# Kernel tuning notes

Measured on AMD Instinct MI355X. Metric: run time of the kernel, lower is better.

Reference implementation:

```python
import jax, jax.numpy as jnp
import numpy as np

N = 100000   # nodes
E = 1000000  # edges
IN, HID, OUT = 128, 64, 64


def setup_inputs() -> dict:
    key = jax.random.key(0)
    ks = jax.random.split(key, 6)
    x = jax.random.normal(ks[0], (N, IN), dtype=jnp.float32)
    edge_index = jax.random.randint(ks[1], (2, E), 0, N, dtype=jnp.int64)
    edge_attr = jax.random.uniform(ks[2], (E,), dtype=jnp.float32)
    # Glorot-style init like PyG GCNConv (weight [in, out], bias zeros)
    W1 = jax.random.normal(ks[3], (IN, HID), dtype=jnp.float32) * (1.0 / np.sqrt(IN))
    b1 = jnp.zeros((HID,), dtype=jnp.float32)
    W2 = jax.random.normal(ks[4], (HID, OUT), dtype=jnp.float32) * (1.0 / np.sqrt(HID))
    b2 = jnp.zeros((OUT,), dtype=jnp.float32)
    return {"x": x, "edge_index": edge_index, "edge_attr": edge_attr,
            "W1": W1, "b1": b1, "W2": W2, "b2": b2}


def gcn_conv(x, edge_index, edge_weight, W, b):
    """GCNConv: add self-loops, symmetric normalization, linear + scatter-add."""
    n = x.shape[0]
    row, col = edge_index[0], edge_index[1]
    loop = jnp.arange(n, dtype=row.dtype)
    row = jnp.concatenate([row, loop])
    col = jnp.concatenate([col, loop])
    w = jnp.concatenate([edge_weight, jnp.ones((n,), dtype=x.dtype)])
    deg = jax.ops.segment_sum(w, col, num_segments=n)              # [N]
    dinv = jnp.where(deg > 0, jax.lax.rsqrt(deg), 0.0)
    norm = dinv[row] * w * dinv[col]                               # [E+N]
    h = x @ W                                                      # [N, out]
    agg = jax.ops.segment_sum(h[row] * norm[:, None], col, num_segments=n)
    return agg + b


def reference(x, edge_index, edge_attr, W1, b1, W2, b2):
    h = jax.nn.relu(gcn_conv(x, edge_index, edge_attr, W1, b1))
    return jax.nn.relu(gcn_conv(h, edge_index, edge_attr, W2, b2))
```

## Files before the change

kernel.cpp:

```cpp
#include <hip/hip_runtime.h>


#define BNODES 512
#define LB 9
#define MAXBKT 256
#define EPT 16
#define EPB (256 * EPT)

typedef __attribute__((ext_vector_type(8))) short bf16x8;
typedef __attribute__((ext_vector_type(8))) unsigned short u16x8;
typedef __attribute__((ext_vector_type(8))) float f32x8;
typedef __attribute__((ext_vector_type(4))) float f32x4;

__device__ __forceinline__ unsigned short f2bf(float f) {
    unsigned u = __float_as_uint(f);
    u = (u + 0x7FFF + ((u >> 16) & 1)) >> 16;
    return (unsigned short)u;
}
__device__ __forceinline__ float bf2f(unsigned short h) {
    return __uint_as_float(((unsigned)h) << 16);
}
__device__ __forceinline__ f32x8 bf8tof(u16x8 u) {
    f32x8 r;
    #pragma unroll
    for (int i = 0; i < 8; ++i) r[i] = bf2f(u[i]);
    return r;
}

__device__ __forceinline__ int waveIncScan(int v, int lane) {
    #pragma unroll
    for (int d = 1; d < 64; d <<= 1) {
        int u = __shfl_up(v, d, 64);
        if (lane >= d) v += u;
    }
    return v;
}

template<int NW>
__device__ __forceinline__ int blockIncScan(int v, int t, int* wt) {
    int lane = t & 63, w = t >> 6;
    int s = waveIncScan(v, lane);
    if (lane == 63) wt[w] = s;
    __syncthreads();
    int add = 0;
    #pragma unroll
    for (int i = 0; i < NW - 1; ++i) if (i < w) add += wt[i];
    return s + add;
}

__device__ __forceinline__ f32x8 gather8(
    const unsigned short* __restrict__ G, const int2* __restrict__ sedge,
    int s, int m, int p8, f32x8 a0)
{
    f32x8 a1 = (f32x8)0.f;
    int e = s, e_end = s + m;
    if ((((unsigned long long)(sedge + e)) & 8) && e < e_end) {
        int2 pk = sedge[e++];
        float w = __int_as_float(pk.y);
        a0 += w * bf8tof(*(const u16x8*)&G[(size_t)pk.x * 64 + p8 * 8]);
    }
    for (; e + 1 < e_end; e += 2) {
        int4 pp = *(const int4*)&sedge[e];
        float w0 = __int_as_float(pp.y);
        float w1 = __int_as_float(pp.w);
        u16x8 g0 = *(const u16x8*)&G[(size_t)pp.x * 64 + p8 * 8];
        u16x8 g1 = *(const u16x8*)&G[(size_t)pp.z * 64 + p8 * 8];
        a0 += w0 * bf8tof(g0);
        a1 += w1 * bf8tof(g1);
    }
    if (e < e_end) {
        int2 pk = sedge[e];
        float w = __int_as_float(pk.y);
        a0 += w * bf8tof(*(const u16x8*)&G[(size_t)pk.x * 64 + p8 * 8]);
    }
    return a0 + a1;
}


__global__ __launch_bounds__(256) void hist_kernel(
    const int* __restrict__ col, int* __restrict__ H, int E, int NBKT,
    const float* __restrict__ W1, const float* __restrict__ W2,
    unsigned short* __restrict__ WT1, unsigned short* __restrict__ WT2, int NEB)
{
    int t = threadIdx.x, blk = blockIdx.x;
    if (blk >= NEB) {
        int i = (blk - NEB) * 256 + t;
        if (i < 64 * 128) {
            int c = i >> 7, k = i & 127;
            WT1[i] = f2bf(W1[k * 64 + c]);
        } else if (i < 64 * 128 + 64 * 64) {
            int j = i - 64 * 128;
            int c = j >> 6, k = j & 63;
            WT2[j] = f2bf(W2[k * 64 + c]);
        }
        return;
    }
    __shared__ int h[MAXBKT];
    for (int b = t; b < NBKT; b += 256) h[b] = 0;
    __syncthreads();
    int base = blk * EPB;
    #pragma unroll
    for (int i = 0; i < EPT; ++i) {
        int e = base + i * 256 + t;
        if (e < E) atomicAdd(&h[col[e] >> LB], 1);
    }
    __syncthreads();
    for (int b = t; b < NBKT; b += 256) H[blk * NBKT + b] = h[b];
}

__global__ __launch_bounds__(256) void rowscan_kernel(
    int* __restrict__ H, int* __restrict__ rowSum, int NEB, int NBKT)
{
    __shared__ int wt[4];
    int b = blockIdx.x, t = threadIdx.x;
    int v = (t < NEB) ? H[t * NBKT + b] : 0;
    int incl = blockIncScan<4>(v, t, wt);
    if (t < NEB) H[t * NBKT + b] = incl - v;
    if (t == 255) rowSum[b] = incl;
}

__global__ __launch_bounds__(256) void bktscan_kernel(
    const int* __restrict__ rowSum, int* __restrict__ bktStart, int NBKT)
{
    __shared__ int wt[4];
    int t = threadIdx.x;
    int v = (t < NBKT) ? rowSum[t] : 0;
    int incl = blockIncScan<4>(v, t, wt);
    if (t < NBKT) bktStart[t] = incl - v;
    if (t == NBKT - 1) bktStart[NBKT] = incl;
}

#define SMEMSZ (EPB * 8 + EPB + MAXBKT * 16 + 32)
__global__ __launch_bounds__(256) void scatter_gemm_kernel(
    const int* __restrict__ row, const int* __restrict__ col,
    const float* __restrict__ w, const int* __restrict__ H,
    const int* __restrict__ bktStart, int2* __restrict__ sedge1,
    int E, int NBKT, int NEB,
    const float* __restrict__ X, const unsigned short* __restrict__ WT,
    unsigned short* __restrict__ G, int n)
{
    __shared__ __align__(16) char smem[SMEMSZ];
    const int t = threadIdx.x;
    const int blk = blockIdx.x;

    if (blk < NEB) {
        int2* stage = (int2*)smem;
        unsigned char* bstage = (unsigned char*)(stage + EPB);
        int* lcnt  = (int*)(bstage + EPB);
        int* loff  = lcnt + MAXBKT;
        int* lcur  = loff + MAXBKT;
        int* gbase = lcur + MAXBKT;
        int* wt    = gbase + MAXBKT;

        for (int b = t; b < NBKT; b += 256) lcnt[b] = 0;
        __syncthreads();
        int base = blk * EPB;
        #pragma unroll
        for (int i = 0; i < EPT; ++i) {
            int e = base + i * 256 + t;
            if (e < E) atomicAdd(&lcnt[col[e] >> LB], 1);
        }
        __syncthreads();
        int v = (t < NBKT) ? lcnt[t] : 0;
        int incl = blockIncScan<4>(v, t, wt);
        if (t < NBKT) {
            int x0 = incl - v;
            loff[t] = x0;
            lcur[t] = x0;
            gbase[t] = bktStart[t] + H[blk * NBKT + t];
        }
        __syncthreads();
        #pragma unroll
        for (int i = 0; i < EPT; ++i) {
            int e = base + i * 256 + t;
            if (e < E) {
                int c = col[e];
                int b = c >> LB;
                int pos = atomicAdd(&lcur[b], 1);
                int2 pk;
                pk.x = row[e] | ((c & (BNODES - 1)) << 20);
                pk.y = __float_as_int(w[e]);
                stage[pos] = pk;
                bstage[pos] = (unsigned char)b;
            }
        }
        __syncthreads();
        int ecnt = E - base; if (ecnt > EPB) ecnt = EPB;
        for (int i = t; i < ecnt; i += 256) {
            int b = bstage[i];
            int g = gbase[b] + (i - loff[b]);
            sedge1[g] = stage[i];
        }
        return;
    }

    constexpr int K = 128, ROWB = 256, SLOTS = 16, CPR = 32;
    char* xs = smem;
    char* ws = smem + 64 * ROWB;
    const int nodeBase = (blk - NEB) * 64;

    for (int q = t; q < 64 * SLOTS; q += 256) {
        int r = q / SLOTS, s = q % SLOTS;
        uint4 v = *(const uint4*)(WT + r * K + s * 8);
        *(uint4*)(ws + r * ROWB + ((s ^ (r & 7)) * 16)) = v;
    }
    for (int q = t; q < 64 * CPR; q += 256) {
        int r = q / CPR, c = q % CPR;
        int node = nodeBase + r;
        float4 v = make_float4(0.f, 0.f, 0.f, 0.f);
        if (node < n) v = *(const float4*)(X + (size_t)node * K + c * 4);
        ushort4 h;
        h.x = f2bf(v.x); h.y = f2bf(v.y); h.z = f2bf(v.z); h.w = f2bf(v.w);
        *(ushort4*)(xs + r * ROWB + (((c >> 1) ^ (r & 7)) * 16) + (c & 1) * 8) = h;
    }
    __syncthreads();

    const int lane = t & 63;
    const int wv = t >> 6;
    const int lr = lane & 15;
    const int lk = lane >> 4;
    const int arow = (wv << 4) + lr;

    f32x4 acc[4] = {};
    #pragma unroll
    for (int kb = 0; kb < 4; ++kb) {
        int s = kb * 4 + lk;
        bf16x8 a = *(bf16x8*)(xs + arow * ROWB + ((s ^ (arow & 7)) * 16));
        #pragma unroll
        for (int cb = 0; cb < 4; ++cb) {
            int c = cb * 16 + lr;
            bf16x8 b = *(bf16x8*)(ws + c * ROWB + ((s ^ (c & 7)) * 16));
            acc[cb] = __builtin_amdgcn_mfma_f32_16x16x32_bf16(a, b, acc[cb], 0, 0, 0);
        }
    }

    int rowbase = nodeBase + (wv << 4) + (lk << 2);
    #pragma unroll
    for (int j = 0; j < 4; ++j) {
        int node = rowbase + j;
        if (node >= n) continue;
        #pragma unroll
        for (int cb = 0; cb < 4; ++cb)
            G[(size_t)node * 64 + cb * 16 + lr] = f2bf(acc[cb][j]);
    }
}

__global__ __launch_bounds__(512) void fine_kernel(
    const int2* __restrict__ sedge1, const int* __restrict__ bktStart,
    int2* __restrict__ sedge2, int* __restrict__ nodeStart,
    int* __restrict__ nodeCnt, float* __restrict__ dinv,
    unsigned short* __restrict__ g1, int n)
{
    __shared__ int cnt[BNODES];
    __shared__ float wsum[BNODES];
    __shared__ int off[BNODES];
    __shared__ int cur[BNODES];
    __shared__ float dloc[BNODES];
    __shared__ int wt[8];
    int b = blockIdx.x, t = threadIdx.x;
    cnt[t] = 0; wsum[t] = 1.0f;
    __syncthreads();
    int s = bktStart[b], e = bktStart[b + 1];
    for (int j = s + t; j < e; j += 512) {
        int2 pk = sedge1[j];
        int ld = pk.x >> 20;
        atomicAdd(&cnt[ld], 1);
        atomicAdd(&wsum[ld], __int_as_float(pk.y));
    }
    __syncthreads();
    int v = cnt[t];
    int incl = blockIncScan<8>(v, t, wt);
    int x0 = s + incl - v;
    off[t] = x0;
    cur[t] = x0;
    dloc[t] = rsqrtf(wsum[t]);
    __syncthreads();
    int node = b * BNODES + t;
    if (node < n) {
        nodeStart[node] = off[t];
        nodeCnt[node] = cnt[t];
        dinv[node] = dloc[t];
    }
    for (int j = s + t; j < e; j += 512) {
        int2 pk = sedge1[j];
        int ld = pk.x >> 20;
        int pos = atomicAdd(&cur[ld], 1);
        sedge2[pos] = make_int2(pk.x & 0xFFFFF, pk.y);
    }
    for (int q = t; q < BNODES * 8; q += 512) {
        int r = q >> 3, cc = q & 7;
        int nd = b * BNODES + r;
        if (nd >= n) continue;
        float dv = dloc[r];
        size_t offb = (size_t)nd * 64 + cc * 8;
        ushort4 u0 = *(const ushort4*)(g1 + offb);
        ushort4 u1 = *(const ushort4*)(g1 + offb + 4);
        u0.x = f2bf(bf2f(u0.x) * dv); u0.y = f2bf(bf2f(u0.y) * dv);
        u0.z = f2bf(bf2f(u0.z) * dv); u0.w = f2bf(bf2f(u0.w) * dv);
        u1.x = f2bf(bf2f(u1.x) * dv); u1.y = f2bf(bf2f(u1.y) * dv);
        u1.z = f2bf(bf2f(u1.z) * dv); u1.w = f2bf(bf2f(u1.w) * dv);
        *(ushort4*)(g1 + offb) = u0;
        *(ushort4*)(g1 + offb + 4) = u1;
    }
}

__global__ __launch_bounds__(256) void aggmm_kernel(
    const unsigned short* __restrict__ G1, const int2* __restrict__ sedge2,
    const int* __restrict__ nodeStart, const int* __restrict__ nodeCnt,
    const float* __restrict__ dinv, const float* __restrict__ bias,
    const unsigned short* __restrict__ WT2, unsigned short* __restrict__ G2, int n)
{
    constexpr int BN = 32;
    constexpr int ROWB = 128;
    __shared__ char smem[(BN + 64) * ROWB];
    char* xs = smem;
    char* ws = smem + BN * ROWB;
    const int tid = threadIdx.x;
    const int nodeBase = blockIdx.x * BN;

    for (int q = tid; q < 64 * 8; q += 256) {
        int r = q >> 3, s = q & 7;
        uint4 v = *(const uint4*)(WT2 + r * 64 + s * 8);
        *(uint4*)(ws + r * ROWB + ((s ^ (r & 7)) * 16)) = v;
    }

    int p8 = tid & 7;
    int r = tid >> 3;
    int node = nodeBase + r;
    f32x8 o = (f32x8)0.f;
    if (node < n) {
        f32x8 a = bf8tof(*(const u16x8*)&G1[(size_t)node * 64 + p8 * 8]);
        a = gather8(G1, sedge2, nodeStart[node], nodeCnt[node], p8, a);
        float di = dinv[node];
        #pragma unroll
        for (int i = 0; i < 8; ++i)
            o[i] = fmaxf(fmaf(di, a[i], bias[p8 * 8 + i]), 0.f);
    }
    u16x8 h;
    #pragma unroll
    for (int i = 0; i < 8; ++i) h[i] = f2bf(o[i]);
    *(u16x8*)(xs + r * ROWB + ((p8 ^ (r & 7)) * 16)) = h;
    __syncthreads();

    const int lane = tid & 63;
    const int w = tid >> 6;
    const int lr = lane & 15;
    const int lk = lane >> 4;
    const int rb = w >> 1;
    const int arow = rb * 16 + lr;

    f32x4 acc[2] = {};
    #pragma unroll
    for (int kb = 0; kb < 2; ++kb) {
        int s = kb * 4 + lk;
        bf16x8 a = *(bf16x8*)(xs + arow * ROWB + ((s ^ (arow & 7)) * 16));
        #pragma unroll
        for (int cc = 0; cc < 2; ++cc) {
            int c = ((w & 1) * 2 + cc) * 16 + lr;
            bf16x8 b = *(bf16x8*)(ws + c * ROWB + ((s ^ (c & 7)) * 16));
            acc[cc] = __builtin_amdgcn_mfma_f32_16x16x32_bf16(a, b, acc[cc], 0, 0, 0);
        }
    }

    int rowbase = nodeBase + rb * 16 + (lk << 2);
    #pragma unroll
    for (int j = 0; j < 4; ++j) {
        int nd = rowbase + j;
        if (nd >= n) continue;
        float dv = dinv[nd];
        #pragma unroll
        for (int cc = 0; cc < 2; ++cc)
            G2[(size_t)nd * 64 + ((w & 1) * 2 + cc) * 16 + lr] = f2bf(acc[cc][j] * dv);
    }
}

__global__ __launch_bounds__(256) void agg_kernel(
    const unsigned short* __restrict__ G, const int2* __restrict__ sedge2,
    const int* __restrict__ nodeStart, const int* __restrict__ nodeCnt,
    const float* __restrict__ dinv, const float* __restrict__ bias,
    float* __restrict__ OUT, int n)
{
    int t = blockIdx.x * blockDim.x + threadIdx.x;
    if (t >= n * 8) return;
    int node = t >> 3, p8 = t & 7;

    f32x8 a = bf8tof(*(const u16x8*)&G[(size_t)node * 64 + p8 * 8]);
    a = gather8(G, sedge2, nodeStart[node], nodeCnt[node], p8, a);

    float di = dinv[node];
    float4 o0, o1;
    o0.x = fmaxf(fmaf(di, a[0], bias[p8 * 8 + 0]), 0.f);
    o0.y = fmaxf(fmaf(di, a[1], bias[p8 * 8 + 1]), 0.f);
    o0.z = fmaxf(fmaf(di, a[2], bias[p8 * 8 + 2]), 0.f);
    o0.w = fmaxf(fmaf(di, a[3], bias[p8 * 8 + 3]), 0.f);
    o1.x = fmaxf(fmaf(di, a[4], bias[p8 * 8 + 4]), 0.f);
    o1.y = fmaxf(fmaf(di, a[5], bias[p8 * 8 + 5]), 0.f);
    o1.z = fmaxf(fmaf(di, a[6], bias[p8 * 8 + 6]), 0.f);
    o1.w = fmaxf(fmaf(di, a[7], bias[p8 * 8 + 7]), 0.f);
    *(float4*)&OUT[(size_t)node * 64 + p8 * 8] = o0;
    *(float4*)&OUT[(size_t)node * 64 + p8 * 8 + 4] = o1;
}

extern "C" void kernel_launch(void* const* d_in, const int* in_sizes, int n_in,
                              void* d_out, int out_size, void* d_ws, size_t ws_size,
                              hipStream_t stream) {
    const float* x     = (const float*)d_in[0];
    const int*   eidx  = (const int*)d_in[1];
    const float* eattr = (const float*)d_in[2];
    const float* W1    = (const float*)d_in[3];
    const float* b1    = (const float*)d_in[4];
    const float* W2    = (const float*)d_in[5];
    const float* b2    = (const float*)d_in[6];
    float* out = (float*)d_out;

    const int n = in_sizes[0] / 128;
    const int E = in_sizes[2];
    const int* row = eidx;
    const int* col = eidx + E;

    const int NBKT = (n + BNODES - 1) / BNODES;
    const int NEB  = (E + EPB - 1) / EPB;

    int2*  sedge1 = (int2*)d_ws;
    int2*  sedge2 = sedge1 + (size_t)E;
    unsigned short* g1 = (unsigned short*)(sedge2 + (size_t)E);
    unsigned short* g2 = g1 + (size_t)n * 64;
    unsigned short* WT1 = g2 + (size_t)n * 64;
    unsigned short* WT2 = WT1 + 64 * 128;
    float* dinv      = (float*)(WT2 + 64 * 64);
    int*   nodeStart = (int*)(dinv + n);
    int*   nodeCnt   = nodeStart + n;
    int*   H         = nodeCnt + n;
    int*   rowSum    = H + (size_t)NEB * NBKT;
    int*   bktStart  = rowSum + NBKT;

    const int nbG  = (n + 63) / 64;
    const int nbG2 = (n + 31) / 32;
    const int nbA8 = (int)(((size_t)n * 8 + 255) / 256);

    hist_kernel<<<NEB + 48, 256, 0, stream>>>(col, H, E, NBKT, W1, W2, WT1, WT2, NEB);
    rowscan_kernel<<<NBKT, 256, 0, stream>>>(H, rowSum, NEB, NBKT);
    bktscan_kernel<<<1, 256, 0, stream>>>(rowSum, bktStart, NBKT);
    scatter_gemm_kernel<<<NEB + nbG, 256, 0, stream>>>(
        row, col, eattr, H, bktStart, sedge1, E, NBKT, NEB, x, WT1, g1, n);
    fine_kernel<<<NBKT, 512, 0, stream>>>(sedge1, bktStart, sedge2, nodeStart,
                                          nodeCnt, dinv, g1, n);

    aggmm_kernel<<<nbG2, 256, 0, stream>>>(g1, sedge2, nodeStart, nodeCnt, dinv, b1, WT2, g2, n);
    agg_kernel<<<nbA8, 256, 0, stream>>>(g2, sedge2, nodeStart, nodeCnt, dinv, b2, out, n);
}
```

Measured before the change: 112.5 us.

## Fold bucket-start scan into consumers and shrink edges per block

Removes the single-block bktscan kernel launch by having scatter_gemm and fine_kernel each recompute the exclusive scan of per-bucket totals locally from rowSum. EPT drops from 16 to 12, which raises the number of edge blocks above 256. Rowscan therefore moves to 512 threads so one block still covers all edge-block counts. The change saves a launch and a dependent serial step, but every block now repeats a small redundant scan and there are more edge blocks to schedule.

```diff
diff --git a/kernel.cpp b/kernel.cpp
--- a/kernel.cpp
+++ b/kernel.cpp
@@ -4,7 +4,7 @@
 #define BNODES 512
 #define LB 9
 #define MAXBKT 256
-#define EPT 16
+#define EPT 12
 #define EPB (256 * EPT)
 
 typedef __attribute__((ext_vector_type(8))) short bf16x8;
@@ -108,38 +108,26 @@
     for (int b = t; b < NBKT; b += 256) H[blk * NBKT + b] = h[b];
 }
 
-__global__ __launch_bounds__(256) void rowscan_kernel(
+__global__ __launch_bounds__(512) void rowscan_kernel(
     int* __restrict__ H, int* __restrict__ rowSum, int NEB, int NBKT)
 {
-    __shared__ int wt[4];
+    __shared__ int wt[8];
     int b = blockIdx.x, t = threadIdx.x;
     int v = (t < NEB) ? H[t * NBKT + b] : 0;
-    int incl = blockIncScan<4>(v, t, wt);
+    int incl = blockIncScan<8>(v, t, wt);
     if (t < NEB) H[t * NBKT + b] = incl - v;
-    if (t == 255) rowSum[b] = incl;
-}
-
-__global__ __launch_bounds__(256) void bktscan_kernel(
-    const int* __restrict__ rowSum, int* __restrict__ bktStart, int NBKT)
-{
-    __shared__ int wt[4];
-    int t = threadIdx.x;
-    int v = (t < NBKT) ? rowSum[t] : 0;
-    int incl = blockIncScan<4>(v, t, wt);
-    if (t < NBKT) bktStart[t] = incl - v;
-    if (t == NBKT - 1) bktStart[NBKT] = incl;
-}
-
-#define SMEMSZ (EPB * 8 + EPB + MAXBKT * 16 + 32)
+    if (t == 511) rowSum[b] = incl;
+}
+
 __global__ __launch_bounds__(256) void scatter_gemm_kernel(
     const int* __restrict__ row, const int* __restrict__ col,
     const float* __restrict__ w, const int* __restrict__ H,
-    const int* __restrict__ bktStart, int2* __restrict__ sedge1,
+    const int* __restrict__ rowSum, int2* __restrict__ sedge1,
     int E, int NBKT, int NEB,
     const float* __restrict__ X, const unsigned short* __restrict__ WT,
     unsigned short* __restrict__ G, int n)
 {
-    __shared__ __align__(16) char smem[SMEMSZ];
+    __shared__ __align__(16) char smem[32768];
     const int t = threadIdx.x;
     const int blk = blockIdx.x;
 
@@ -152,8 +140,12 @@
         int* gbase = lcur + MAXBKT;
         int* wt    = gbase + MAXBKT;
 
+        int vb = (t < NBKT) ? rowSum[t] : 0;
+        int ib = blockIncScan<4>(vb, t, wt);
+        if (t < NBKT) gbase[t] = (ib - vb) + H[blk * NBKT + t];
         for (int b = t; b < NBKT; b += 256) lcnt[b] = 0;
         __syncthreads();
+
         int base = blk * EPB;
         #pragma unroll
         for (int i = 0; i < EPT; ++i) {
@@ -167,7 +159,6 @@
             int x0 = incl - v;
             loff[t] = x0;
             lcur[t] = x0;
-            gbase[t] = bktStart[t] + H[blk * NBKT + t];
         }
         __syncthreads();
         #pragma unroll
@@ -246,21 +237,28 @@
 }
 
 __global__ __launch_bounds__(512) void fine_kernel(
-    const int2* __restrict__ sedge1, const int* __restrict__ bktStart,
+    const int2* __restrict__ sedge1, const int* __restrict__ rowSum,
     int2* __restrict__ sedge2, int* __restrict__ nodeStart,
     int* __restrict__ nodeCnt, float* __restrict__ dinv,
-    unsigned short* __restrict__ g1, int n)
+    unsigned short* __restrict__ g1, int n, int NBKT)
 {
     __shared__ int cnt[BNODES];
     __shared__ float wsum[BNODES];
     __shared__ int off[BNODES];
     __shared__ int cur[BNODES];
     __shared__ float dloc[BNODES];
+    __shared__ int bs[MAXBKT + 1];
     __shared__ int wt[8];
     int b = blockIdx.x, t = threadIdx.x;
+
+    int vb = (t < NBKT) ? rowSum[t] : 0;
+    int ib = blockIncScan<8>(vb, t, wt);
+    if (t < NBKT) bs[t] = ib - vb;
+    if (t == 511) bs[NBKT] = ib;
     cnt[t] = 0; wsum[t] = 1.0f;
     __syncthreads();
-    int s = bktStart[b], e = bktStart[b + 1];
+
+    int s = bs[b], e = (b + 1 <= NBKT) ? bs[b + 1] : bs[NBKT];
     for (int j = s + t; j < e; j += 512) {
         int2 pk = sedge1[j];
         int ld = pk.x >> 20;
@@ -432,19 +430,17 @@
     int*   nodeCnt   = nodeStart + n;
     int*   H         = nodeCnt + n;
     int*   rowSum    = H + (size_t)NEB * NBKT;
-    int*   bktStart  = rowSum + NBKT;
 
     const int nbG  = (n + 63) / 64;
     const int nbG2 = (n + 31) / 32;
     const int nbA8 = (int)(((size_t)n * 8 + 255) / 256);
 
     hist_kernel<<<NEB + 48, 256, 0, stream>>>(col, H, E, NBKT, W1, W2, WT1, WT2, NEB);
-    rowscan_kernel<<<NBKT, 256, 0, stream>>>(H, rowSum, NEB, NBKT);
-    bktscan_kernel<<<1, 256, 0, stream>>>(rowSum, bktStart, NBKT);
+    rowscan_kernel<<<NBKT, 512, 0, stream>>>(H, rowSum, NEB, NBKT);
     scatter_gemm_kernel<<<NEB + nbG, 256, 0, stream>>>(
-        row, col, eattr, H, bktStart, sedge1, E, NBKT, NEB, x, WT1, g1, n);
-    fine_kernel<<<NBKT, 512, 0, stream>>>(sedge1, bktStart, sedge2, nodeStart,
-                                          nodeCnt, dinv, g1, n);
+        row, col, eattr, H, rowSum, sedge1, E, NBKT, NEB, x, WT1, g1, n);
+    fine_kernel<<<NBKT, 512, 0, stream>>>(sedge1, rowSum, sedge2, nodeStart,
+                                          nodeCnt, dinv, g1, n, NBKT);
 
     aggmm_kernel<<<nbG2, 256, 0, stream>>>(g1, sedge2, nodeStart, nodeCnt, dinv, b1, WT2, g2, n);
     agg_kernel<<<nbA8, 256, 0, stream>>>(g2, sedge2, nodeStart, nodeCnt, dinv, b2, out, n);
```

After: 108.9 us. 3.2% less time.
